# Kernel optimization log

Hardware: AMD Instinct MI355X
Metric: run time of the kernel (lower is better)

## Reference

```python
import jax, jax.numpy as jnp
import numpy as np

EMBED_DIM = 1024
NUM_HEADS = 16
HEAD_DIM = EMBED_DIM // NUM_HEADS


def setup_inputs() -> dict:
    key = jax.random.key(0)
    ks = jax.random.split(key, 5)
    B, S, D = 2, 2048, EMBED_DIM
    scale = 1.0 / np.sqrt(D)
    x = jax.random.normal(ks[0], (B, S, D), dtype=jnp.float32)
    qkv_w = jax.random.uniform(ks[1], (3 * D, D), dtype=jnp.float32, minval=-scale, maxval=scale)
    qkv_b = jax.random.uniform(ks[2], (3 * D,), dtype=jnp.float32, minval=-scale, maxval=scale)
    out_w = jax.random.uniform(ks[3], (D, D), dtype=jnp.float32, minval=-scale, maxval=scale)
    out_b = jax.random.uniform(ks[4], (D,), dtype=jnp.float32, minval=-scale, maxval=scale)
    return {"x": x, "qkv_w": qkv_w, "qkv_b": qkv_b, "out_w": out_w, "out_b": out_b}


def reference(x, qkv_w, qkv_b, out_w, out_b):
    B, S, D = x.shape
    H, hd = NUM_HEADS, HEAD_DIM
    # QKV projection (torch Linear: y = x @ W^T + b)
    qkv = jnp.einsum('bsd,ed->bse', x, qkv_w) + qkv_b          # [B,S,3D]
    qkv = qkv.reshape(B, S, 3, H, hd)
    q, k, v = (jnp.moveaxis(qkv[:, :, i], 2, 1) for i in range(3))  # each [B,H,S,hd]
    scores = jnp.einsum('bhqd,bhkd->bhqk', q, k) / np.sqrt(hd)  # [B,H,S,S]
    probs = jax.nn.softmax(scores, axis=-1)
    attn = jnp.einsum('bhqk,bhkd->bhqd', probs, v)              # [B,H,S,hd]
    attn = jnp.moveaxis(attn, 1, 2).reshape(B, S, D)
    return jnp.einsum('bsd,ed->bse', attn, out_w) + out_b
```

## Files before the change

### kernel.cpp

```cpp
#include <hip/hip_runtime.h>
#include <stdint.h>

typedef __bf16 bf16;
typedef __attribute__((ext_vector_type(2))) __bf16 bf16x2;
typedef __attribute__((ext_vector_type(4))) __bf16 bf16x4;
typedef __attribute__((ext_vector_type(8))) __bf16 bf16x8;
typedef __attribute__((ext_vector_type(4))) float f32x4;
typedef __attribute__((ext_vector_type(16))) float f32x16;

#define LOG2E_OVER_8 0.18033688011112042f

#if __has_builtin(__builtin_amdgcn_exp2f)
#define EXP2(x) __builtin_amdgcn_exp2f(x)
#else
#define EXP2(x) exp2f(x)
#endif

__device__ __forceinline__ void gl_lds16(const bf16* g, bf16* l) {
  __builtin_amdgcn_global_load_lds(
      (const __attribute__((address_space(1))) void*)g,
      (__attribute__((address_space(3))) void*)l, 16, 0, 0);
}
#define WAIT_VM0_BARRIER() asm volatile("s_waitcnt vmcnt(0)\n\ts_barrier" ::: "memory")

__device__ __forceinline__ uint32_t pack2(float a, float b) {
  union { bf16x2 v; uint32_t u; } z;
  z.v[0] = (bf16)a; z.v[1] = (bf16)b;
  return z.u;
}

#define N_X  (4096 * 1024)
#define N_WQ (3072 * 1024)
#define N_WO (1024 * 1024)
__global__ __launch_bounds__(256) void cvt3_kernel(const float* __restrict__ x,
                                                   const float* __restrict__ wq,
                                                   const float* __restrict__ wo,
                                                   bf16* __restrict__ d) {
  int i = (blockIdx.x * 256 + threadIdx.x) * 8;
  const float* s;
  if (i < N_X) s = x + i;
  else if (i < N_X + N_WQ) s = wq + (i - N_X);
  else s = wo + (i - N_X - N_WQ);
  float4 a = *(const float4*)s;
  float4 b = *(const float4*)(s + 4);
  bf16x8 o;
  o[0] = (bf16)a.x; o[1] = (bf16)a.y; o[2] = (bf16)a.z; o[3] = (bf16)a.w;
  o[4] = (bf16)b.x; o[5] = (bf16)b.y; o[6] = (bf16)b.z; o[7] = (bf16)b.w;
  *(bf16x8*)(d + i) = o;
}

template <int EPI>
__global__ __launch_bounds__(256, 3) void gemm_bt(
    const bf16* __restrict__ A, const bf16* __restrict__ Bw,
    const float* __restrict__ bias,
    bf16* __restrict__ qo, bf16* __restrict__ ko, bf16* __restrict__ vTo,
    float* __restrict__ outF) {
  constexpr int MT = EPI ? 64 : 128;
  constexpr int MI = MT / 32;
  constexpr int BK = EPI ? 64 : 32;
  constexpr int NC = BK / 32;
  constexpr int NIT = 1024 / BK;
  constexpr int ASZ = MT * BK;
  constexpr int BSZ = 128 * BK;
  constexpr int RS = 136;
  constexpr int SME0 = 2 * ASZ + 2 * BSZ;
  constexpr int SME = EPI ? SME0 : (SME0 > 128 * RS ? SME0 : 128 * RS);
  __shared__ __attribute__((aligned(16))) bf16 smem[SME];

  int bx, by;
  {
    const int f = blockIdx.x;
    const int xcd = f & 7, idx = f >> 3;
    if constexpr (EPI == 0) { by = xcd * 4 + (idx & 3); bx = idx >> 2; }
    else                    { by = xcd * 8 + (idx & 7); bx = idx >> 3; }
  }

  const int t = threadIdx.x;
  const int L = t & 63;
  const int li = L & 15;
  const int qd = L >> 4;
  const int w = t >> 6;
  const int wm = (w >> 1) * (MT / 2);
  const int wn = (w & 1) * 64;
  const int bm0 = by * MT;
  const int bn0 = bx * 128;
  const int r_st = t >> 2;
  const int c_st = (t & 3) * 8;

  const bf16* Ab = A + (size_t)bm0 * 1024;
  const bf16* Bb = Bw + (size_t)bn0 * 1024;

  auto issue = [&](int k0, int bi) {
    bf16* As_ = smem + bi * ASZ;
    bf16* Bs_ = smem + 2 * ASZ + bi * BSZ;
#pragma unroll
    for (int kc = 0; kc < NC; ++kc) {
      const int kk = k0 + kc * 32;
      gl_lds16(Ab + (size_t)r_st * 1024 + kk + c_st, As_ + kc * MT * 32 + t * 8);
      if constexpr (MT == 128)
        gl_lds16(Ab + (size_t)(r_st + 64) * 1024 + kk + c_st,
                 As_ + kc * MT * 32 + (t + 256) * 8);
      gl_lds16(Bb + (size_t)r_st * 1024 + kk + c_st, Bs_ + kc * 4096 + t * 8);
      gl_lds16(Bb + (size_t)(r_st + 64) * 1024 + kk + c_st,
               Bs_ + kc * 4096 + (t + 256) * 8);
    }
  };

  f32x4 acc[MI][4] = {};
  issue(0, 0);
  for (int it = 0; it < NIT; ++it) {
    WAIT_VM0_BARRIER();
    if (it < NIT - 1) issue((it + 1) * BK, (it + 1) & 1);
    const bf16* Ac = smem + (it & 1) * ASZ;
    const bf16* Bc = smem + 2 * ASZ + (it & 1) * BSZ;
#pragma unroll
    for (int kc = 0; kc < NC; ++kc) {
      const bf16* Ak = Ac + kc * MT * 32;
      const bf16* Bk = Bc + kc * 4096;
      bf16x8 af[MI], bfr[4];
#pragma unroll
      for (int mi = 0; mi < MI; ++mi)
        af[mi] = *(const bf16x8*)(Ak + (wm + mi * 16 + li) * 32 + qd * 8);
#pragma unroll
      for (int ni = 0; ni < 4; ++ni)
        bfr[ni] = *(const bf16x8*)(Bk + (wn + ni * 16 + li) * 32 + qd * 8);
#pragma unroll
      for (int mi = 0; mi < MI; ++mi)
#pragma unroll
        for (int ni = 0; ni < 4; ++ni)
          acc[mi][ni] = __builtin_amdgcn_mfma_f32_16x16x32_bf16(
              af[mi], bfr[ni], acc[mi][ni], 0, 0, 0);
    }
  }

  if constexpr (EPI == 0) {
    const int which = bn0 >> 10;
    __syncthreads();
    bf16* Ct = smem;
    if (which == 2) {
#pragma unroll
      for (int mi = 0; mi < MI; ++mi) {
        const int m_l = wm + mi * 16 + qd * 4;
#pragma unroll
        for (int ni = 0; ni < 4; ++ni) {
          const int n_l = wn + ni * 16 + li;
          const float bi = bias[bn0 + n_l];
          bf16x4 pk;
#pragma unroll
          for (int r = 0; r < 4; ++r) pk[r] = (bf16)(acc[mi][ni][r] + bi);
          *(bf16x4*)(Ct + n_l * RS + m_l) = pk;
        }
      }
    } else {
      const float sc = (which == 0) ? LOG2E_OVER_8 : 1.0f;
#pragma unroll
      for (int mi = 0; mi < MI; ++mi) {
        const int m_l = wm + mi * 16 + qd * 4;
#pragma unroll
        for (int ni = 0; ni < 4; ++ni) {
          const int n_l = wn + ni * 16 + li;
          const float bi = bias[bn0 + n_l];
#pragma unroll
          for (int r = 0; r < 4; ++r)
            Ct[(m_l + r) * RS + n_l] = (bf16)((acc[mi][ni][r] + bi) * sc);
        }
      }
    }
    __syncthreads();
    const int jr = t >> 4;
    const int jc = t & 15;
#pragma unroll
    for (int pass = 0; pass < 8; ++pass) {
      const int row = pass * 16 + jr;
      bf16x8 vv = *(const bf16x8*)(Ct + row * RS + jc * 8);
      if (which == 2) {
        const int n_g = bn0 + row;
        const int hh = (n_g >> 6) & 15, dd = n_g & 63;
        const int bb = bm0 >> 11;
        const int s_b = (bm0 & 2047) + jc * 8;
        *(bf16x8*)(vTo + ((size_t)(bb * 16 + hh) * 64 + dd) * 2048 + s_b) = vv;
      } else {
        const int m_g = bm0 + row;
        const int bb = m_g >> 11, ss = m_g & 2047;
        const int n_g = bn0 + jc * 8;
        const int hh = (n_g >> 6) & 15, dd = n_g & 63;
        bf16* dst = (which == 0 ? qo : ko);
        *(bf16x8*)(dst + ((size_t)(bb * 16 + hh) * 2048 + ss) * 64 + dd) = vv;
      }
    }
  } else {
#pragma unroll
    for (int mi = 0; mi < MI; ++mi) {
      const int m_g = bm0 + wm + mi * 16 + qd * 4;
#pragma unroll
      for (int ni = 0; ni < 4; ++ni) {
        const int n_g = bn0 + wn + ni * 16 + li;
        const float bi = bias[n_g];
#pragma unroll
        for (int r = 0; r < 4; ++r)
          outF[(size_t)(m_g + r) * 1024 + n_g] = acc[mi][ni][r] + bi;
      }
    }
  }
}

__global__ __launch_bounds__(256, 2) void attn_fwd(
    const bf16* __restrict__ Q, const bf16* __restrict__ K,
    const bf16* __restrict__ VT, bf16* __restrict__ AO) {
  __shared__ __attribute__((aligned(16))) bf16 Ks[2 * 8192];
  __shared__ __attribute__((aligned(16))) bf16 Vs[2 * 8192];
  const int t = threadIdx.x;
  const int L = t & 63;
  const int m31 = L & 31;
  const int hi = L >> 5;
  const int w = t >> 6;

  const int lid = blockIdx.x;
  const int bh_ = ((lid & 7) << 2) + (lid >> 7);
  const int qb = (lid >> 3) & 15;
  const int b = bh_ >> 4, h = bh_ & 15;
  const size_t bh = (size_t)(b * 16 + h);

  const bf16* Qp = Q + bh * 2048 * 64;
  const bf16* Kp = K + bh * 2048 * 64;
  const bf16* Vp = VT + bh * 64 * 2048;
  const int q0 = qb * 128 + w * 32;

  bf16x8 qf[4];
#pragma unroll
  for (int s = 0; s < 4; ++s)
    qf[s] = *(const bf16x8*)(Qp + (size_t)(q0 + m31) * 64 + s * 16 + hi * 8);

  f32x16 acc[2] = {};
  float lsum = 0.f;

  const int srow = t >> 3;
  const int scc = (t & 7) ^ (srow & 7);
  auto issue = [&](int it2, int bi) {
#pragma unroll
    for (int tile = 0; tile < 2; ++tile) {
      const int kt = it2 * 2 + tile;
      const bf16* Kt = Kp + (size_t)kt * 4096;
      const bf16* Vt = Vp + kt * 64;
      bf16* Kd = Ks + bi * 8192 + tile * 4096;
      bf16* Vd = Vs + bi * 8192 + tile * 4096;
#pragma unroll
      for (int r = 0; r < 2; ++r) {
        gl_lds16(Kt + (srow + 32 * r) * 64 + scc * 8, Kd + (t + 256 * r) * 8);
        gl_lds16(Vt + (size_t)(srow + 32 * r) * 2048 + scc * 8, Vd + (t + 256 * r) * 8);
      }
    }
  };

  const int rlow = m31 & 7;
  issue(0, 0);
  for (int it2 = 0; it2 < 16; ++it2) {
    WAIT_VM0_BARRIER();
    if (it2 < 15) issue(it2 + 1, (it2 + 1) & 1);
#pragma unroll
    for (int tile = 0; tile < 2; ++tile) {
      const bf16* Kc = Ks + (it2 & 1) * 8192 + tile * 4096;
      const bf16* Vc = Vs + (it2 & 1) * 8192 + tile * 4096;

      f32x16 st[2];
#pragma unroll
      for (int kt2 = 0; kt2 < 2; ++kt2) {
        f32x16 z = {};
#pragma unroll
        for (int s = 0; s < 4; ++s) {
          bf16x8 kf = *(const bf16x8*)(
              Kc + ((kt2 * 32 + m31) * 8 + ((2 * s + hi) ^ rlow)) * 8);
          z = __builtin_amdgcn_mfma_f32_32x32x16_bf16(kf, qf[s], z, 0, 0, 0);
        }
        st[kt2] = z;
      }

      uint32_t pk[2][8];
#pragma unroll
      for (int kt2 = 0; kt2 < 2; ++kt2)
#pragma unroll
        for (int j = 0; j < 8; ++j) {
          float a = EXP2(st[kt2][2 * j]);
          float c = EXP2(st[kt2][2 * j + 1]);
          lsum += a + c;
          pk[kt2][j] = pack2(a, c);
        }

      uint32_t sw[2][8];
#pragma unroll
      for (int kt2 = 0; kt2 < 2; ++kt2)
#pragma unroll
        for (int j = 0; j < 8; ++j)
          sw[kt2][j] = (uint32_t)__shfl_xor((int)pk[kt2][j], 32);

      union FU { uint32_t u[4]; bf16x8 v; };
      FU af[2][2];
#pragma unroll
      for (int kt2 = 0; kt2 < 2; ++kt2) {
        if (hi == 0) {
          af[kt2][0].u[0] = pk[kt2][0]; af[kt2][0].u[1] = pk[kt2][1];
          af[kt2][0].u[2] = sw[kt2][0]; af[kt2][0].u[3] = sw[kt2][1];
          af[kt2][1].u[0] = pk[kt2][4]; af[kt2][1].u[1] = pk[kt2][5];
          af[kt2][1].u[2] = sw[kt2][4]; af[kt2][1].u[3] = sw[kt2][5];
        } else {
          af[kt2][0].u[0] = sw[kt2][2]; af[kt2][0].u[1] = sw[kt2][3];
          af[kt2][0].u[2] = pk[kt2][2]; af[kt2][0].u[3] = pk[kt2][3];
          af[kt2][1].u[0] = sw[kt2][6]; af[kt2][1].u[1] = sw[kt2][7];
          af[kt2][1].u[2] = pk[kt2][6]; af[kt2][1].u[3] = pk[kt2][7];
        }
      }

#pragma unroll
      for (int dt = 0; dt < 2; ++dt)
#pragma unroll
        for (int kt2 = 0; kt2 < 2; ++kt2)
#pragma unroll
          for (int u = 0; u < 2; ++u) {
            bf16x8 vf = *(const bf16x8*)(
                Vc + ((dt * 32 + m31) * 8 + ((kt2 * 4 + u * 2 + hi) ^ rlow)) * 8);
            acc[dt] = __builtin_amdgcn_mfma_f32_32x32x16_bf16(af[kt2][u].v, vf,
                                                              acc[dt], 0, 0, 0);
          }
    }
  }

  lsum += __shfl_xor(lsum, 32);
  const float inv = 1.f / lsum;

#pragma unroll
  for (int r = 0; r < 16; ++r) {
    const int qrow = (r & 3) + 8 * (r >> 2) + 4 * hi;
    const float invq = __shfl(inv, qrow);
    const size_t base = ((size_t)b * 2048 + q0 + qrow) * 1024 + h * 64 + m31;
    AO[base] = (bf16)(acc[0][r] * invq);
    AO[base + 32] = (bf16)(acc[1][r] * invq);
  }
}

extern "C" void kernel_launch(void* const* d_in, const int* in_sizes, int n_in,
                              void* d_out, int out_size, void* d_ws, size_t ws_size,
                              hipStream_t stream) {
  const float* x = (const float*)d_in[0];
  const float* qkvw = (const float*)d_in[1];
  const float* qkvb = (const float*)d_in[2];
  const float* outw = (const float*)d_in[3];
  const float* outb = (const float*)d_in[4];
  float* out = (float*)d_out;

  bf16* xb = (bf16*)d_ws;
  bf16* wq = xb + (size_t)N_X;
  bf16* wo = wq + (size_t)N_WQ;
  bf16* q = wo + (size_t)N_WO;
  bf16* kk = q + (size_t)2 * 16 * 2048 * 64;
  bf16* vT = kk + (size_t)2 * 16 * 2048 * 64;
  bf16* attn = xb;

  cvt3_kernel<<<4096, 256, 0, stream>>>(x, qkvw, outw, xb);

  gemm_bt<0><<<768, 256, 0, stream>>>(xb, wq, qkvb, q, kk, vT, nullptr);
  attn_fwd<<<512, 256, 0, stream>>>(q, kk, vT, attn);
  gemm_bt<1><<<512, 256, 0, stream>>>(attn, wo, outb, nullptr, nullptr, nullptr, out);
}
```

Measured before the change: 177.8 us.

## Use permlane32 swap for P transpose and batch both tiles per iteration

```diff
diff --git a/kernel.cpp b/kernel.cpp
--- a/kernel.cpp
+++ b/kernel.cpp
@@ -27,6 +27,10 @@
   union { bf16x2 v; uint32_t u; } z;
   z.v[0] = (bf16)a; z.v[1] = (bf16)b;
   return z.u;
+}
+
+__device__ __forceinline__ void pl32swap(uint32_t& a, uint32_t& b) {
+  asm("v_permlane32_swap_b32 %0, %1" : "+v"(a), "+v"(b));
 }
 
 #define N_X  (4096 * 1024)
@@ -231,8 +235,8 @@
   for (int s = 0; s < 4; ++s)
     qf[s] = *(const bf16x8*)(Qp + (size_t)(q0 + m31) * 64 + s * 16 + hi * 8);
 
-  f32x16 acc[2] = {};
-  float lsum = 0.f;
+  f32x16 acc[2][2] = {};
+  float ls[4] = {0.f, 0.f, 0.f, 0.f};
 
   const int srow = t >> 3;
   const int scc = (t & 7) ^ (srow & 7);
@@ -257,12 +261,13 @@
   for (int it2 = 0; it2 < 16; ++it2) {
     WAIT_VM0_BARRIER();
     if (it2 < 15) issue(it2 + 1, (it2 + 1) & 1);
+    const bf16* Kc0 = Ks + (it2 & 1) * 8192;
+    const bf16* Vc0 = Vs + (it2 & 1) * 8192;
+
+    f32x16 st[2][2];
 #pragma unroll
     for (int tile = 0; tile < 2; ++tile) {
-      const bf16* Kc = Ks + (it2 & 1) * 8192 + tile * 4096;
-      const bf16* Vc = Vs + (it2 & 1) * 8192 + tile * 4096;
-
-      f32x16 st[2];
+      const bf16* Kc = Kc0 + tile * 4096;
 #pragma unroll
       for (int kt2 = 0; kt2 < 2; ++kt2) {
         f32x16 z = {};
@@ -272,58 +277,57 @@
               Kc + ((kt2 * 32 + m31) * 8 + ((2 * s + hi) ^ rlow)) * 8);
           z = __builtin_amdgcn_mfma_f32_32x32x16_bf16(kf, qf[s], z, 0, 0, 0);
         }
-        st[kt2] = z;
-      }
-
-      uint32_t pk[2][8];
-#pragma unroll
-      for (int kt2 = 0; kt2 < 2; ++kt2)
+        st[tile][kt2] = z;
+      }
+    }
+
+    union FU { uint32_t u[4]; bf16x8 v; };
+    FU af[2][2][2];
+#pragma unroll
+    for (int tile = 0; tile < 2; ++tile)
+#pragma unroll
+      for (int kt2 = 0; kt2 < 2; ++kt2) {
+        uint32_t pk[8];
+        float lsl = 0.f;
 #pragma unroll
         for (int j = 0; j < 8; ++j) {
-          float a = EXP2(st[kt2][2 * j]);
-          float c = EXP2(st[kt2][2 * j + 1]);
-          lsum += a + c;
-          pk[kt2][j] = pack2(a, c);
+          float a = EXP2(st[tile][kt2][2 * j]);
+          float c = EXP2(st[tile][kt2][2 * j + 1]);
+          lsl += a + c;
+          pk[j] = pack2(a, c);
         }
-
-      uint32_t sw[2][8];
-#pragma unroll
-      for (int kt2 = 0; kt2 < 2; ++kt2)
-#pragma unroll
-        for (int j = 0; j < 8; ++j)
-          sw[kt2][j] = (uint32_t)__shfl_xor((int)pk[kt2][j], 32);
-
-      union FU { uint32_t u[4]; bf16x8 v; };
-      FU af[2][2];
-#pragma unroll
-      for (int kt2 = 0; kt2 < 2; ++kt2) {
-        if (hi == 0) {
-          af[kt2][0].u[0] = pk[kt2][0]; af[kt2][0].u[1] = pk[kt2][1];
-          af[kt2][0].u[2] = sw[kt2][0]; af[kt2][0].u[3] = sw[kt2][1];
-          af[kt2][1].u[0] = pk[kt2][4]; af[kt2][1].u[1] = pk[kt2][5];
-          af[kt2][1].u[2] = sw[kt2][4]; af[kt2][1].u[3] = sw[kt2][5];
-        } else {
-          af[kt2][0].u[0] = sw[kt2][2]; af[kt2][0].u[1] = sw[kt2][3];
-          af[kt2][0].u[2] = pk[kt2][2]; af[kt2][0].u[3] = pk[kt2][3];
-          af[kt2][1].u[0] = sw[kt2][6]; af[kt2][1].u[1] = sw[kt2][7];
-          af[kt2][1].u[2] = pk[kt2][6]; af[kt2][1].u[3] = pk[kt2][7];
-        }
-      }
-
-#pragma unroll
-      for (int dt = 0; dt < 2; ++dt)
+        ls[tile * 2 + kt2] += lsl;
+        pl32swap(pk[0], pk[2]);
+        pl32swap(pk[1], pk[3]);
+        pl32swap(pk[4], pk[6]);
+        pl32swap(pk[5], pk[7]);
+        af[tile][kt2][0].u[0] = pk[0]; af[tile][kt2][0].u[1] = pk[1];
+        af[tile][kt2][0].u[2] = pk[2]; af[tile][kt2][0].u[3] = pk[3];
+        af[tile][kt2][1].u[0] = pk[4]; af[tile][kt2][1].u[1] = pk[5];
+        af[tile][kt2][1].u[2] = pk[6]; af[tile][kt2][1].u[3] = pk[7];
+      }
+
+#pragma unroll
+    for (int dt = 0; dt < 2; ++dt)
+#pragma unroll
+      for (int tile = 0; tile < 2; ++tile) {
+        const bf16* Vc = Vc0 + tile * 4096;
 #pragma unroll
         for (int kt2 = 0; kt2 < 2; ++kt2)
 #pragma unroll
           for (int u = 0; u < 2; ++u) {
             bf16x8 vf = *(const bf16x8*)(
                 Vc + ((dt * 32 + m31) * 8 + ((kt2 * 4 + u * 2 + hi) ^ rlow)) * 8);
-            acc[dt] = __builtin_amdgcn_mfma_f32_32x32x16_bf16(af[kt2][u].v, vf,
-                                                              acc[dt], 0, 0, 0);
+            acc[dt][tile] = __builtin_amdgcn_mfma_f32_32x32x16_bf16(
+                af[tile][kt2][u].v, vf, acc[dt][tile], 0, 0, 0);
           }
-    }
-  }
-
+      }
+  }
+
+  f32x16 accf[2];
+#pragma unroll
+  for (int dt = 0; dt < 2; ++dt) accf[dt] = acc[dt][0] + acc[dt][1];
+  float lsum = (ls[0] + ls[1]) + (ls[2] + ls[3]);
   lsum += __shfl_xor(lsum, 32);
   const float inv = 1.f / lsum;
 
@@ -332,8 +336,8 @@
     const int qrow = (r & 3) + 8 * (r >> 2) + 4 * hi;
     const float invq = __shfl(inv, qrow);
     const size_t base = ((size_t)b * 2048 + q0 + qrow) * 1024 + h * 64 + m31;
-    AO[base] = (bf16)(acc[0][r] * invq);
-    AO[base + 32] = (bf16)(acc[1][r] * invq);
+    AO[base] = (bf16)(accf[0][r] * invq);
+    AO[base + 32] = (bf16)(accf[1][r] * invq);
   }
 }
 
```

After: 176.5 us. No clear change (-0.7%).
